# Kernel optimization log

Measured on AMD Instinct MI355X. Metric: run time of the kernel, lower is better.

The kernel has to match this reference:

```python
import jax, jax.numpy as jnp
import numpy as np

NHEAD = 8
D_MODEL = 256
B, L, NB = 16, 8192, 8


def setup_inputs() -> dict:
    key = jax.random.key(0)
    ks = jax.random.split(key, 8)
    x = jax.random.normal(ks[0], (B, L, D_MODEL), dtype=jnp.float32)
    mask = jax.random.randint(ks[1], (B, L), 0, 2) == 1  # bool, True = valid
    backend_id = jax.random.randint(ks[2], (B, L), 0, NB).astype(jnp.int32)
    query = 0.02 * jax.random.normal(ks[3], (1, 1, D_MODEL), dtype=jnp.float32)
    in_proj_weight = 0.02 * jax.random.normal(ks[4], (3 * D_MODEL, D_MODEL), dtype=jnp.float32)
    in_proj_bias = jnp.zeros((3 * D_MODEL,), dtype=jnp.float32)
    out_proj_weight = 0.02 * jax.random.normal(ks[5], (D_MODEL, D_MODEL), dtype=jnp.float32)
    out_proj_bias = jnp.zeros((D_MODEL,), dtype=jnp.float32)
    ln_gamma = jnp.ones((D_MODEL,), dtype=jnp.float32)
    ln_beta = jnp.zeros((D_MODEL,), dtype=jnp.float32)
    return {
        "x": x,
        "query": query,
        "in_proj_weight": in_proj_weight,
        "in_proj_bias": in_proj_bias,
        "out_proj_weight": out_proj_weight,
        "out_proj_bias": out_proj_bias,
        "ln_gamma": ln_gamma,
        "ln_beta": ln_beta,
        "mask": mask,
        "backend_id": backend_id,
        "n_backends_max": NB,
    }


def reference(x, query, in_proj_weight, in_proj_bias, out_proj_weight,
              out_proj_bias, ln_gamma, ln_beta, mask, backend_id, n_backends_max):
    Bs, Ls, D = x.shape
    H = NHEAD
    hd = D // H
    # Split packed torch in_proj into q/k/v projections.
    wq, wk, wv = jnp.split(in_proj_weight, 3, axis=0)
    bq, bk, bv = jnp.split(in_proj_bias, 3, axis=0)
    # Shared single query projected once (same for every batch/backend).
    q = (query[0, 0] @ wq.T + bq).reshape(H, hd)            # (H, hd)
    k = (x @ wk.T + bk).reshape(Bs, Ls, H, hd)              # (B, L, H, hd)
    v = (x @ wv.T + bv).reshape(Bs, Ls, H, hd)              # (B, L, H, hd)
    scores = jnp.einsum("hd,blhd->bhl", q, k) / jnp.sqrt(jnp.float32(hd))
    # Per-backend masks, vectorized over the backend axis n.
    b_ids = jnp.arange(n_backends_max, dtype=backend_id.dtype)
    b_mask = mask[None] & (backend_id[None] == b_ids[:, None, None])  # (NB, B, L)
    has_tokens = b_mask.any(axis=-1)                                   # (NB, B)
    safe_mask = jnp.where(has_tokens[:, :, None], b_mask, mask[None])  # fall back to full mask
    logits = jnp.where(safe_mask[:, :, None, :], scores[None], jnp.float32(-1e9))  # (NB,B,H,L)
    w = jax.nn.softmax(logits, axis=-1)
    ctx = jnp.einsum("nbhl,blhd->nbhd", w, v).reshape(n_backends_max, Bs, D)
    out = ctx @ out_proj_weight.T + out_proj_bias            # (NB, B, D)
    # LayerNorm over last dim.
    mu = out.mean(axis=-1, keepdims=True)
    var = out.var(axis=-1, keepdims=True)
    out = (out - mu) * jax.lax.rsqrt(var + 1e-5) * ln_gamma + ln_beta
    # Zero contexts for backends with no tokens.
    out = out * has_tokens[:, :, None].astype(out.dtype)
    return jnp.transpose(out, (1, 0, 2))                     # (B, NB, D)
```

## Files before the change

### kernel.cpp

```cpp
#include <hip/hip_runtime.h>
#include <cstdint>
#include <cstddef>

#define B_  16
#define L_  8192
#define D_  256
#define H_  8
#define NB_ 8

static const long OFF_QK   = 0;
static const long OFF_QB   = 2048;
static const long OFF_PART = 4096;

__global__ __launch_bounds__(256) void k_setup(const float* __restrict__ query,
                                               const float* __restrict__ W,
                                               const float* __restrict__ bias,
                                               float* __restrict__ ws) {
    __shared__ float q_s[256];
    int t = threadIdx.x;
    int h = blockIdx.x;
    float acc = bias[t];
    const float* wr = W + (long)t * 256;
    #pragma unroll 8
    for (int e = 0; e < 256; e += 4) {
        float4 qv = *(const float4*)(query + e);
        float4 wv = *(const float4*)(wr + e);
        acc += qv.x * wv.x + qv.y * wv.y + qv.z * wv.z + qv.w * wv.w;
    }
    q_s[t] = acc;
    __syncthreads();
    const float rs = 0.17677669529663687f;
    float s = 0.f;
    #pragma unroll 8
    for (int d = 0; d < 32; ++d) {
        int r = 256 + h * 32 + d;
        s += q_s[h * 32 + d] * W[(long)r * 256 + t];
    }
    ws[OFF_QK + h * 256 + t] = s * rs;
    if (t < 64) {
        float v = (t < 32) ? q_s[h * 32 + t] * bias[256 + h * 32 + t] : 0.f;
        v += __shfl_down(v, 16);
        v += __shfl_down(v, 8);
        v += __shfl_down(v, 4);
        v += __shfl_down(v, 2);
        v += __shfl_down(v, 1);
        if (t == 0) ws[OFF_QB + h] = v * rs;
    }
}

__device__ __forceinline__ float reduce_ep(float p0, float p1, float p2, float p3,
                                           float p4, float p5, float p6, float p7, int ep) {
    bool b1 = (ep & 1) != 0;
    float s0 = b1 ? p0 : p1, k0 = b1 ? p1 : p0;
    float s1 = b1 ? p2 : p3, k1 = b1 ? p3 : p2;
    float s2 = b1 ? p4 : p5, k2 = b1 ? p5 : p4;
    float s3 = b1 ? p6 : p7, k3 = b1 ? p7 : p6;
    float n0 = k0 + __shfl_xor(s0, 1);
    float n1 = k1 + __shfl_xor(s1, 1);
    float n2 = k2 + __shfl_xor(s2, 1);
    float n3 = k3 + __shfl_xor(s3, 1);
    bool b2 = (ep & 2) != 0;
    float t0s = b2 ? n0 : n1, t0k = b2 ? n1 : n0;
    float t1s = b2 ? n2 : n3, t1k = b2 ? n3 : n2;
    float m0 = t0k + __shfl_xor(t0s, 2);
    float m1 = t1k + __shfl_xor(t1s, 2);
    bool b4 = (ep & 4) != 0;
    float us = b4 ? m0 : m1, uk = b4 ? m1 : m0;
    return uk + __shfl_xor(us, 4);
}

template <int NCH>
__global__ __launch_bounds__(256) void k_pool(const float* __restrict__ x,
                                              const unsigned char* __restrict__ mask,
                                              const int* __restrict__ bid,
                                              const float* __restrict__ ws,
                                              float* __restrict__ part,
                                              float* __restrict__ pse) {
    const int CH = L_ / NCH;
    const int WLEN = CH / 4;
    __shared__ float red[4 * 2048];
    __shared__ float rse[4 * 8];

    int t = threadIdx.x;
    int widx = t >> 6, lane = t & 63;
    int ep = lane & 7;

    int blk = blockIdx.x;
    int b  = blk / (NB_ * NCH);
    int n  = (blk / NCH) % NB_;
    int ch = blk % NCH;

    const float* xb = x + (long)b * L_ * D_;
    const int*   bb = bid + (long)b * L_;

    float4 qk0 = *(const float4*)(ws + OFF_QK + 0 * 256 + lane * 4);
    float4 qk1 = *(const float4*)(ws + OFF_QK + 1 * 256 + lane * 4);
    float4 qk2 = *(const float4*)(ws + OFF_QK + 2 * 256 + lane * 4);
    float4 qk3 = *(const float4*)(ws + OFF_QK + 3 * 256 + lane * 4);
    float4 qk4 = *(const float4*)(ws + OFF_QK + 4 * 256 + lane * 4);
    float4 qk5 = *(const float4*)(ws + OFF_QK + 5 * 256 + lane * 4);
    float4 qk6 = *(const float4*)(ws + OFF_QK + 6 * 256 + lane * 4);
    float4 qk7 = *(const float4*)(ws + OFF_QK + 7 * 256 + lane * 4);
    float qbreg = ws[OFF_QB + ep];

    const int* mi = (const int*)mask;
    bool bytemode = __ballot((unsigned)mi[lane] > 1u) != 0ull;
    const unsigned char* mb_byte = mask + (long)b * L_;
    const int* mb_int = mi + (long)b * L_;

    float4 acc[8];
    #pragma unroll
    for (int h = 0; h < 8; ++h) acc[h] = make_float4(0.f, 0.f, 0.f, 0.f);
    float se = 0.f;

    int l0 = ch * CH + widx * WLEN;
    for (int w0 = l0; w0 < l0 + WLEN; w0 += 64) {
        int l = w0 + lane;
        bool valid = bytemode ? (mb_byte[l] != 0) : (mb_int[l] != 0);
        bool m = valid && (bb[l] == n);
        unsigned long long bal = __ballot(m);
        while (bal) {
            int i0 = __ffsll(bal) - 1; bal &= bal - 1;
            int i1 = -1;
            if (bal) { i1 = __ffsll(bal) - 1; bal &= bal - 1; }
            int tokA = w0 + i0;
            int tokB = w0 + (i1 >= 0 ? i1 : i0);
            float gB = (i1 >= 0) ? 1.f : 0.f;
            float4 xa = ((const float4*)(xb + (long)tokA * D_))[lane];
            float4 xc = ((const float4*)(xb + (long)tokB * D_))[lane];
            float pA0 = xa.x*qk0.x + xa.y*qk0.y + xa.z*qk0.z + xa.w*qk0.w;
            float pA1 = xa.x*qk1.x + xa.y*qk1.y + xa.z*qk1.z + xa.w*qk1.w;
            float pA2 = xa.x*qk2.x + xa.y*qk2.y + xa.z*qk2.z + xa.w*qk2.w;
            float pA3 = xa.x*qk3.x + xa.y*qk3.y + xa.z*qk3.z + xa.w*qk3.w;
            float pA4 = xa.x*qk4.x + xa.y*qk4.y + xa.z*qk4.z + xa.w*qk4.w;
            float pA5 = xa.x*qk5.x + xa.y*qk5.y + xa.z*qk5.z + xa.w*qk5.w;
            float pA6 = xa.x*qk6.x + xa.y*qk6.y + xa.z*qk6.z + xa.w*qk6.w;
            float pA7 = xa.x*qk7.x + xa.y*qk7.y + xa.z*qk7.z + xa.w*qk7.w;
            float pB0 = xc.x*qk0.x + xc.y*qk0.y + xc.z*qk0.z + xc.w*qk0.w;
            float pB1 = xc.x*qk1.x + xc.y*qk1.y + xc.z*qk1.z + xc.w*qk1.w;
            float pB2 = xc.x*qk2.x + xc.y*qk2.y + xc.z*qk2.z + xc.w*qk2.w;
            float pB3 = xc.x*qk3.x + xc.y*qk3.y + xc.z*qk3.z + xc.w*qk3.w;
            float pB4 = xc.x*qk4.x + xc.y*qk4.y + xc.z*qk4.z + xc.w*qk4.w;
            float pB5 = xc.x*qk5.x + xc.y*qk5.y + xc.z*qk5.z + xc.w*qk5.w;
            float pB6 = xc.x*qk6.x + xc.y*qk6.y + xc.z*qk6.z + xc.w*qk6.w;
            float pB7 = xc.x*qk7.x + xc.y*qk7.y + xc.z*qk7.z + xc.w*qk7.w;
            float sA = reduce_ep(pA0, pA1, pA2, pA3, pA4, pA5, pA6, pA7, ep);
            float sB = reduce_ep(pB0, pB1, pB2, pB3, pB4, pB5, pB6, pB7, ep);
            sA += __shfl_xor(sA, 8);  sB += __shfl_xor(sB, 8);
            sA += __shfl_xor(sA, 16); sB += __shfl_xor(sB, 16);
            sA += __shfl_xor(sA, 32); sB += __shfl_xor(sB, 32);
            float wA = __expf(sA + qbreg);
            float wB = __expf(sB + qbreg) * gB;
            se += wA + wB;
            {
                float a = __shfl(wA, 0), c = __shfl(wB, 0);
                acc[0].x += a*xa.x + c*xc.x; acc[0].y += a*xa.y + c*xc.y;
                acc[0].z += a*xa.z + c*xc.z; acc[0].w += a*xa.w + c*xc.w;
            }
            {
                float a = __shfl(wA, 1), c = __shfl(wB, 1);
                acc[1].x += a*xa.x + c*xc.x; acc[1].y += a*xa.y + c*xc.y;
                acc[1].z += a*xa.z + c*xc.z; acc[1].w += a*xa.w + c*xc.w;
            }
            {
                float a = __shfl(wA, 2), c = __shfl(wB, 2);
                acc[2].x += a*xa.x + c*xc.x; acc[2].y += a*xa.y + c*xc.y;
                acc[2].z += a*xa.z + c*xc.z; acc[2].w += a*xa.w + c*xc.w;
            }
            {
                float a = __shfl(wA, 3), c = __shfl(wB, 3);
                acc[3].x += a*xa.x + c*xc.x; acc[3].y += a*xa.y + c*xc.y;
                acc[3].z += a*xa.z + c*xc.z; acc[3].w += a*xa.w + c*xc.w;
            }
            {
                float a = __shfl(wA, 4), c = __shfl(wB, 4);
                acc[4].x += a*xa.x + c*xc.x; acc[4].y += a*xa.y + c*xc.y;
                acc[4].z += a*xa.z + c*xc.z; acc[4].w += a*xa.w + c*xc.w;
            }
            {
                float a = __shfl(wA, 5), c = __shfl(wB, 5);
                acc[5].x += a*xa.x + c*xc.x; acc[5].y += a*xa.y + c*xc.y;
                acc[5].z += a*xa.z + c*xc.z; acc[5].w += a*xa.w + c*xc.w;
            }
            {
                float a = __shfl(wA, 6), c = __shfl(wB, 6);
                acc[6].x += a*xa.x + c*xc.x; acc[6].y += a*xa.y + c*xc.y;
                acc[6].z += a*xa.z + c*xc.z; acc[6].w += a*xa.w + c*xc.w;
            }
            {
                float a = __shfl(wA, 7), c = __shfl(wB, 7);
                acc[7].x += a*xa.x + c*xc.x; acc[7].y += a*xa.y + c*xc.y;
                acc[7].z += a*xa.z + c*xc.z; acc[7].w += a*xa.w + c*xc.w;
            }
        }
    }

    #pragma unroll
    for (int h = 0; h < 8; ++h)
        *(float4*)(red + widx * 2048 + h * 256 + lane * 4) = acc[h];
    if (lane < 8) rse[widx * 8 + lane] = se;
    __syncthreads();
    long base = (long)blk * 2048;
    for (int idx = t; idx < 2048; idx += 256) {
        float s = red[idx] + red[2048 + idx] + red[4096 + idx] + red[6144 + idx];
        part[base + idx] = s;
    }
    if (t < 8) pse[(long)blk * 8 + t] = rse[t] + rse[8 + t] + rse[16 + t] + rse[24 + t];
}

template <int NCH>
__global__ __launch_bounds__(256) void k_epi(const float* __restrict__ part,
                                             const float* __restrict__ pse,
                                             const float* __restrict__ W,
                                             const float* __restrict__ ib,
                                             const float* __restrict__ Wo,
                                             const float* __restrict__ ob,
                                             const float* __restrict__ gamma,
                                             const float* __restrict__ beta,
                                             float* __restrict__ out) {
    __shared__ float pn[2048];
    __shared__ float ses[8];
    __shared__ float ctx_s[256];
    __shared__ float r1[4], r2[4];
    int n = blockIdx.x & 7, b = blockIdx.x >> 3;
    int t = threadIdx.x;
    int tbase = b * (NB_ * NCH) + n * NCH;
    if (t < 8) {
        float s = 0.f;
        for (int sub = 0; sub < NCH; ++sub) s += pse[(long)(tbase + sub) * 8 + t];
        ses[t] = s;
    }
    __syncthreads();
    bool has = ses[0] > 0.f;
    for (int j = 0; j < 8; ++j) {
        int idx = j * 256 + t;
        int h = idx >> 8;
        float s = 0.f;
        for (int sub = 0; sub < NCH; ++sub) s += part[(long)(tbase + sub) * 2048 + idx];
        pn[idx] = has ? s / ses[h] : 0.f;
    }
    __syncthreads();
    int h = t >> 5;
    float c = ib[512 + t];
    {
        const float* wr = W + (long)(512 + t) * 256;
        const float* ph = pn + h * 256;
        for (int e = 0; e < 256; e += 4) {
            float4 wv4 = *(const float4*)(wr + e);
            float4 pv4 = *(const float4*)(ph + e);
            c += wv4.x * pv4.x + wv4.y * pv4.y + wv4.z * pv4.z + wv4.w * pv4.w;
        }
    }
    ctx_s[t] = c;
    __syncthreads();
    float o = ob[t];
    {
        const float* wr = Wo + (long)t * 256;
        for (int d = 0; d < 256; d += 4) {
            float4 wv4 = *(const float4*)(wr + d);
            float4 cv4 = *(const float4*)(ctx_s + d);
            o += wv4.x * cv4.x + wv4.y * cv4.y + wv4.z * cv4.z + wv4.w * cv4.w;
        }
    }
    float s1 = o, s2 = o * o;
    #pragma unroll
    for (int off = 32; off >= 1; off >>= 1) {
        s1 += __shfl_down(s1, off);
        s2 += __shfl_down(s2, off);
    }
    if ((t & 63) == 0) { r1[t >> 6] = s1; r2[t >> 6] = s2; }
    __syncthreads();
    float S1 = r1[0] + r1[1] + r1[2] + r1[3];
    float S2 = r2[0] + r2[1] + r2[2] + r2[3];
    float mu = S1 * (1.f / 256.f);
    float var = S2 * (1.f / 256.f) - mu * mu;
    float rr = rsqrtf(var + 1e-5f);
    float res = ((o - mu) * rr * gamma[t] + beta[t]) * (has ? 1.f : 0.f);
    out[((long)b * 8 + n) * 256 + t] = res;
}

extern "C" void kernel_launch(void* const* d_in, const int* in_sizes, int n_in,
                              void* d_out, int out_size, void* d_ws, size_t ws_size,
                              hipStream_t stream) {
    const float* x     = (const float*)d_in[0];
    const float* query = (const float*)d_in[1];
    const float* W     = (const float*)d_in[2];
    const float* ib    = (const float*)d_in[3];
    const float* Wo    = (const float*)d_in[4];
    const float* ob    = (const float*)d_in[5];
    const float* gamma = (const float*)d_in[6];
    const float* beta  = (const float*)d_in[7];
    const unsigned char* mask = (const unsigned char*)d_in[8];
    const int* bid     = (const int*)d_in[9];
    float* out = (float*)d_out;
    float* ws  = (float*)d_ws;

    k_setup<<<8, 256, 0, stream>>>(query, W, ib, ws);

    auto need = [](long nch) {
        return (size_t)(OFF_PART + (long)B_ * NB_ * nch * (2048 + 8)) * sizeof(float);
    };
    float* part = ws + OFF_PART;
    if (ws_size >= need(16)) {
        const int NCH = 16;
        float* pse = part + (long)B_ * NB_ * NCH * 2048;
        k_pool<NCH><<<B_ * NB_ * NCH, 256, 0, stream>>>(x, mask, bid, ws, part, pse);
        k_epi<NCH><<<B_ * NB_, 256, 0, stream>>>(part, pse, W, ib, Wo, ob, gamma, beta, out);
    } else if (ws_size >= need(4)) {
        const int NCH = 4;
        float* pse = part + (long)B_ * NB_ * NCH * 2048;
        k_pool<NCH><<<B_ * NB_ * NCH, 256, 0, stream>>>(x, mask, bid, ws, part, pse);
        k_epi<NCH><<<B_ * NB_, 256, 0, stream>>>(part, pse, W, ib, Wo, ob, gamma, beta, out);
    } else {
        const int NCH = 1;
        float* pse = part + (long)B_ * NB_ * NCH * 2048;
        k_pool<NCH><<<B_ * NB_ * NCH, 256, 0, stream>>>(x, mask, bid, ws, part, pse);
        k_epi<NCH><<<B_ * NB_, 256, 0, stream>>>(part, pse, W, ib, Wo, ob, gamma, beta, out);
    }
}
```

Baseline: 68.39 us.

## Compact per-backend token lists via count/scan/fill before pooled gather

Result: slower. 73.62 us (+7.7%).

```diff
diff --git a/kernel.cpp b/kernel.cpp
--- a/kernel.cpp
+++ b/kernel.cpp
@@ -5,12 +5,16 @@
 #define B_  16
 #define L_  8192
 #define D_  256
-#define H_  8
 #define NB_ 8
+#define NW_ 128
 
 static const long OFF_QK   = 0;
 static const long OFF_QB   = 2048;
-static const long OFF_PART = 4096;
+static const long OFF_CNT  = 4096;
+static const long OFF_OFFS = 20480;
+static const long OFF_TOT  = 36864;
+static const long OFF_CIDX = 36992;
+static const long OFF_PART = 168064;
 
 __global__ __launch_bounds__(256) void k_setup(const float* __restrict__ query,
                                                const float* __restrict__ W,
@@ -45,6 +49,80 @@
         v += __shfl_down(v, 2);
         v += __shfl_down(v, 1);
         if (t == 0) ws[OFF_QB + h] = v * rs;
+    }
+}
+
+__global__ __launch_bounds__(256) void k_count(const unsigned char* __restrict__ mask,
+                                               const int* __restrict__ bid,
+                                               int* __restrict__ cnt) {
+    int widx = threadIdx.x >> 6, lane = threadIdx.x & 63;
+    int gw = blockIdx.x * 4 + widx;
+    int b = gw >> 7, w = gw & 127;
+    const int* mi = (const int*)mask;
+    bool bytemode = __ballot((unsigned)mi[lane] > 1u) != 0ull;
+    int tok = w * 64 + lane;
+    long gl = (long)b * L_ + tok;
+    bool valid = bytemode ? (mask[gl] != 0) : (mi[gl] != 0);
+    int nl = valid ? bid[gl] : NB_;
+    #pragma unroll
+    for (int n = 0; n < NB_; ++n) {
+        unsigned long long bn = __ballot(nl == n);
+        if (lane == n) cnt[(b * NB_ + n) * NW_ + w] = __popcll(bn);
+    }
+}
+
+__global__ __launch_bounds__(256) void k_scan(const int* __restrict__ cnt,
+                                              int* __restrict__ offs,
+                                              int* __restrict__ tot) {
+    __shared__ int c[16384];
+    __shared__ int sums[256];
+    int t = threadIdx.x;
+    for (int i = t; i < 16384; i += 256) c[i] = cnt[i];
+    __syncthreads();
+    int s = 0;
+    int base0 = t * 64;
+    for (int j = 0; j < 64; ++j) s += c[base0 + j];
+    sums[t] = s;
+    __syncthreads();
+    for (int st = 1; st < 256; st <<= 1) {
+        int v = (t >= st) ? sums[t - st] : 0;
+        __syncthreads();
+        sums[t] += v;
+        __syncthreads();
+    }
+    int run = sums[t] - s;
+    for (int j = 0; j < 64; ++j) {
+        offs[base0 + j] = run;
+        run += c[base0 + j];
+    }
+    if (t < 128) {
+        int hi = sums[2 * t + 1];
+        int lo = (t > 0) ? sums[2 * t - 1] : 0;
+        tot[t] = hi - lo;
+    }
+}
+
+__global__ __launch_bounds__(256) void k_fill(const unsigned char* __restrict__ mask,
+                                              const int* __restrict__ bid,
+                                              const int* __restrict__ offs,
+                                              int* __restrict__ cidx) {
+    int widx = threadIdx.x >> 6, lane = threadIdx.x & 63;
+    int gw = blockIdx.x * 4 + widx;
+    int b = gw >> 7, w = gw & 127;
+    const int* mi = (const int*)mask;
+    bool bytemode = __ballot((unsigned)mi[lane] > 1u) != 0ull;
+    int tok = w * 64 + lane;
+    long gl = (long)b * L_ + tok;
+    bool valid = bytemode ? (mask[gl] != 0) : (mi[gl] != 0);
+    int nl = valid ? bid[gl] : NB_;
+    unsigned long long ltmask = (1ull << lane) - 1ull;
+    #pragma unroll
+    for (int n = 0; n < NB_; ++n) {
+        unsigned long long bn = __ballot(nl == n);
+        if (nl == n) {
+            int ord = __popcll(bn & ltmask);
+            cidx[offs[(b * NB_ + n) * NW_ + w] + ord] = tok;
+        }
     }
 }
 
@@ -70,28 +148,33 @@
 }
 
 template <int NCH>
-__global__ __launch_bounds__(256) void k_pool(const float* __restrict__ x,
-                                              const unsigned char* __restrict__ mask,
-                                              const int* __restrict__ bid,
-                                              const float* __restrict__ ws,
-                                              float* __restrict__ part,
-                                              float* __restrict__ pse) {
-    const int CH = L_ / NCH;
-    const int WLEN = CH / 4;
+__global__ __launch_bounds__(256) void k_gather(const float* __restrict__ x,
+                                                const int* __restrict__ offs,
+                                                const int* __restrict__ tot,
+                                                const int* __restrict__ cidx,
+                                                const float* __restrict__ ws,
+                                                float* __restrict__ part,
+                                                float* __restrict__ pse) {
     __shared__ float red[4 * 2048];
     __shared__ float rse[4 * 8];
-
     int t = threadIdx.x;
     int widx = t >> 6, lane = t & 63;
     int ep = lane & 7;
 
     int blk = blockIdx.x;
-    int b  = blk / (NB_ * NCH);
-    int n  = (blk / NCH) % NB_;
+    int b = blk / (NB_ * NCH);
+    int n = (blk / NCH) % NB_;
     int ch = blk % NCH;
+    int bn = b * NB_ + n;
+    int start = offs[bn * NW_];
+    int cnt = tot[bn];
+    int c0 = start + (int)((long)cnt * ch / NCH);
+    int c1 = start + (int)((long)cnt * (ch + 1) / NCH);
+    int len = c1 - c0;
+    int w0 = c0 + (len * widx) / 4;
+    int w1 = c0 + (len * (widx + 1)) / 4;
 
     const float* xb = x + (long)b * L_ * D_;
-    const int*   bb = bid + (long)b * L_;
 
     float4 qk0 = *(const float4*)(ws + OFF_QK + 0 * 256 + lane * 4);
     float4 qk1 = *(const float4*)(ws + OFF_QK + 1 * 256 + lane * 4);
@@ -103,95 +186,81 @@
     float4 qk7 = *(const float4*)(ws + OFF_QK + 7 * 256 + lane * 4);
     float qbreg = ws[OFF_QB + ep];
 
-    const int* mi = (const int*)mask;
-    bool bytemode = __ballot((unsigned)mi[lane] > 1u) != 0ull;
-    const unsigned char* mb_byte = mask + (long)b * L_;
-    const int* mb_int = mi + (long)b * L_;
-
     float4 acc[8];
     #pragma unroll
     for (int h = 0; h < 8; ++h) acc[h] = make_float4(0.f, 0.f, 0.f, 0.f);
     float se = 0.f;
 
-    int l0 = ch * CH + widx * WLEN;
-    for (int w0 = l0; w0 < l0 + WLEN; w0 += 64) {
-        int l = w0 + lane;
-        bool valid = bytemode ? (mb_byte[l] != 0) : (mb_int[l] != 0);
-        bool m = valid && (bb[l] == n);
-        unsigned long long bal = __ballot(m);
-        while (bal) {
-            int i0 = __ffsll(bal) - 1; bal &= bal - 1;
-            int i1 = -1;
-            if (bal) { i1 = __ffsll(bal) - 1; bal &= bal - 1; }
-            int tokA = w0 + i0;
-            int tokB = w0 + (i1 >= 0 ? i1 : i0);
-            float gB = (i1 >= 0) ? 1.f : 0.f;
-            float4 xa = ((const float4*)(xb + (long)tokA * D_))[lane];
-            float4 xc = ((const float4*)(xb + (long)tokB * D_))[lane];
-            float pA0 = xa.x*qk0.x + xa.y*qk0.y + xa.z*qk0.z + xa.w*qk0.w;
-            float pA1 = xa.x*qk1.x + xa.y*qk1.y + xa.z*qk1.z + xa.w*qk1.w;
-            float pA2 = xa.x*qk2.x + xa.y*qk2.y + xa.z*qk2.z + xa.w*qk2.w;
-            float pA3 = xa.x*qk3.x + xa.y*qk3.y + xa.z*qk3.z + xa.w*qk3.w;
-            float pA4 = xa.x*qk4.x + xa.y*qk4.y + xa.z*qk4.z + xa.w*qk4.w;
-            float pA5 = xa.x*qk5.x + xa.y*qk5.y + xa.z*qk5.z + xa.w*qk5.w;
-            float pA6 = xa.x*qk6.x + xa.y*qk6.y + xa.z*qk6.z + xa.w*qk6.w;
-            float pA7 = xa.x*qk7.x + xa.y*qk7.y + xa.z*qk7.z + xa.w*qk7.w;
-            float pB0 = xc.x*qk0.x + xc.y*qk0.y + xc.z*qk0.z + xc.w*qk0.w;
-            float pB1 = xc.x*qk1.x + xc.y*qk1.y + xc.z*qk1.z + xc.w*qk1.w;
-            float pB2 = xc.x*qk2.x + xc.y*qk2.y + xc.z*qk2.z + xc.w*qk2.w;
-            float pB3 = xc.x*qk3.x + xc.y*qk3.y + xc.z*qk3.z + xc.w*qk3.w;
-            float pB4 = xc.x*qk4.x + xc.y*qk4.y + xc.z*qk4.z + xc.w*qk4.w;
-            float pB5 = xc.x*qk5.x + xc.y*qk5.y + xc.z*qk5.z + xc.w*qk5.w;
-            float pB6 = xc.x*qk6.x + xc.y*qk6.y + xc.z*qk6.z + xc.w*qk6.w;
-            float pB7 = xc.x*qk7.x + xc.y*qk7.y + xc.z*qk7.z + xc.w*qk7.w;
-            float sA = reduce_ep(pA0, pA1, pA2, pA3, pA4, pA5, pA6, pA7, ep);
-            float sB = reduce_ep(pB0, pB1, pB2, pB3, pB4, pB5, pB6, pB7, ep);
-            sA += __shfl_xor(sA, 8);  sB += __shfl_xor(sB, 8);
-            sA += __shfl_xor(sA, 16); sB += __shfl_xor(sB, 16);
-            sA += __shfl_xor(sA, 32); sB += __shfl_xor(sB, 32);
-            float wA = __expf(sA + qbreg);
-            float wB = __expf(sB + qbreg) * gB;
-            se += wA + wB;
-            {
-                float a = __shfl(wA, 0), c = __shfl(wB, 0);
-                acc[0].x += a*xa.x + c*xc.x; acc[0].y += a*xa.y + c*xc.y;
-                acc[0].z += a*xa.z + c*xc.z; acc[0].w += a*xa.w + c*xc.w;
-            }
-            {
-                float a = __shfl(wA, 1), c = __shfl(wB, 1);
-                acc[1].x += a*xa.x + c*xc.x; acc[1].y += a*xa.y + c*xc.y;
-                acc[1].z += a*xa.z + c*xc.z; acc[1].w += a*xa.w + c*xc.w;
-            }
-            {
-                float a = __shfl(wA, 2), c = __shfl(wB, 2);
-                acc[2].x += a*xa.x + c*xc.x; acc[2].y += a*xa.y + c*xc.y;
-                acc[2].z += a*xa.z + c*xc.z; acc[2].w += a*xa.w + c*xc.w;
-            }
-            {
-                float a = __shfl(wA, 3), c = __shfl(wB, 3);
-                acc[3].x += a*xa.x + c*xc.x; acc[3].y += a*xa.y + c*xc.y;
-                acc[3].z += a*xa.z + c*xc.z; acc[3].w += a*xa.w + c*xc.w;
-            }
-            {
-                float a = __shfl(wA, 4), c = __shfl(wB, 4);
-                acc[4].x += a*xa.x + c*xc.x; acc[4].y += a*xa.y + c*xc.y;
-                acc[4].z += a*xa.z + c*xc.z; acc[4].w += a*xa.w + c*xc.w;
-            }
-            {
-                float a = __shfl(wA, 5), c = __shfl(wB, 5);
-                acc[5].x += a*xa.x + c*xc.x; acc[5].y += a*xa.y + c*xc.y;
-                acc[5].z += a*xa.z + c*xc.z; acc[5].w += a*xa.w + c*xc.w;
-            }
-            {
-                float a = __shfl(wA, 6), c = __shfl(wB, 6);
-                acc[6].x += a*xa.x + c*xc.x; acc[6].y += a*xa.y + c*xc.y;
-                acc[6].z += a*xa.z + c*xc.z; acc[6].w += a*xa.w + c*xc.w;
-            }
-            {
-                float a = __shfl(wA, 7), c = __shfl(wB, 7);
-                acc[7].x += a*xa.x + c*xc.x; acc[7].y += a*xa.y + c*xc.y;
-                acc[7].z += a*xa.z + c*xc.z; acc[7].w += a*xa.w + c*xc.w;
-            }
+    for (int i = w0; i < w1; i += 2) {
+        int tokA = cidx[i];
+        bool hasB = (i + 1) < w1;
+        int tokB = cidx[hasB ? i + 1 : i];
+        float gB = hasB ? 1.f : 0.f;
+        float4 xa = ((const float4*)(xb + (long)tokA * D_))[lane];
+        float4 xc = ((const float4*)(xb + (long)tokB * D_))[lane];
+        float pA0 = xa.x*qk0.x + xa.y*qk0.y + xa.z*qk0.z + xa.w*qk0.w;
+        float pA1 = xa.x*qk1.x + xa.y*qk1.y + xa.z*qk1.z + xa.w*qk1.w;
+        float pA2 = xa.x*qk2.x + xa.y*qk2.y + xa.z*qk2.z + xa.w*qk2.w;
+        float pA3 = xa.x*qk3.x + xa.y*qk3.y + xa.z*qk3.z + xa.w*qk3.w;
+        float pA4 = xa.x*qk4.x + xa.y*qk4.y + xa.z*qk4.z + xa.w*qk4.w;
+        float pA5 = xa.x*qk5.x + xa.y*qk5.y + xa.z*qk5.z + xa.w*qk5.w;
+        float pA6 = xa.x*qk6.x + xa.y*qk6.y + xa.z*qk6.z + xa.w*qk6.w;
+        float pA7 = xa.x*qk7.x + xa.y*qk7.y + xa.z*qk7.z + xa.w*qk7.w;
+        float pB0 = xc.x*qk0.x + xc.y*qk0.y + xc.z*qk0.z + xc.w*qk0.w;
+        float pB1 = xc.x*qk1.x + xc.y*qk1.y + xc.z*qk1.z + xc.w*qk1.w;
+        float pB2 = xc.x*qk2.x + xc.y*qk2.y + xc.z*qk2.z + xc.w*qk2.w;
+        float pB3 = xc.x*qk3.x + xc.y*qk3.y + xc.z*qk3.z + xc.w*qk3.w;
+        float pB4 = xc.x*qk4.x + xc.y*qk4.y + xc.z*qk4.z + xc.w*qk4.w;
+        float pB5 = xc.x*qk5.x + xc.y*qk5.y + xc.z*qk5.z + xc.w*qk5.w;
+        float pB6 = xc.x*qk6.x + xc.y*qk6.y + xc.z*qk6.z + xc.w*qk6.w;
+        float pB7 = xc.x*qk7.x + xc.y*qk7.y + xc.z*qk7.z + xc.w*qk7.w;
+        float sA = reduce_ep(pA0, pA1, pA2, pA3, pA4, pA5, pA6, pA7, ep);
+        float sB = reduce_ep(pB0, pB1, pB2, pB3, pB4, pB5, pB6, pB7, ep);
+        sA += __shfl_xor(sA, 8);  sB += __shfl_xor(sB, 8);
+        sA += __shfl_xor(sA, 16); sB += __shfl_xor(sB, 16);
+        sA += __shfl_xor(sA, 32); sB += __shfl_xor(sB, 32);
+        float wA = __expf(sA + qbreg);
+        float wB = __expf(sB + qbreg) * gB;
+        se += wA + wB;
+        {
+            float a = __shfl(wA, 0), c = __shfl(wB, 0);
+            acc[0].x += a*xa.x + c*xc.x; acc[0].y += a*xa.y + c*xc.y;
+            acc[0].z += a*xa.z + c*xc.z; acc[0].w += a*xa.w + c*xc.w;
+        }
+        {
+            float a = __shfl(wA, 1), c = __shfl(wB, 1);
+            acc[1].x += a*xa.x + c*xc.x; acc[1].y += a*xa.y + c*xc.y;
+            acc[1].z += a*xa.z + c*xc.z; acc[1].w += a*xa.w + c*xc.w;
+        }
+        {
+            float a = __shfl(wA, 2), c = __shfl(wB, 2);
+            acc[2].x += a*xa.x + c*xc.x; acc[2].y += a*xa.y + c*xc.y;
+            acc[2].z += a*xa.z + c*xc.z; acc[2].w += a*xa.w + c*xc.w;
+        }
+        {
+            float a = __shfl(wA, 3), c = __shfl(wB, 3);
+            acc[3].x += a*xa.x + c*xc.x; acc[3].y += a*xa.y + c*xc.y;
+            acc[3].z += a*xa.z + c*xc.z; acc[3].w += a*xa.w + c*xc.w;
+        }
+        {
+            float a = __shfl(wA, 4), c = __shfl(wB, 4);
+            acc[4].x += a*xa.x + c*xc.x; acc[4].y += a*xa.y + c*xc.y;
+            acc[4].z += a*xa.z + c*xc.z; acc[4].w += a*xa.w + c*xc.w;
+        }
+        {
+            float a = __shfl(wA, 5), c = __shfl(wB, 5);
+            acc[5].x += a*xa.x + c*xc.x; acc[5].y += a*xa.y + c*xc.y;
+            acc[5].z += a*xa.z + c*xc.z; acc[5].w += a*xa.w + c*xc.w;
+        }
+        {
+            float a = __shfl(wA, 6), c = __shfl(wB, 6);
+            acc[6].x += a*xa.x + c*xc.x; acc[6].y += a*xa.y + c*xc.y;
+            acc[6].z += a*xa.z + c*xc.z; acc[6].w += a*xa.w + c*xc.w;
+        }
+        {
+            float a = __shfl(wA, 7), c = __shfl(wB, 7);
+            acc[7].x += a*xa.x + c*xc.x; acc[7].y += a*xa.y + c*xc.y;
+            acc[7].z += a*xa.z + c*xc.z; acc[7].w += a*xa.w + c*xc.w;
         }
     }
 
@@ -294,27 +363,28 @@
     const int* bid     = (const int*)d_in[9];
     float* out = (float*)d_out;
     float* ws  = (float*)d_ws;
+    int*   wsI = (int*)d_ws;
 
     k_setup<<<8, 256, 0, stream>>>(query, W, ib, ws);
+    k_count<<<512, 256, 0, stream>>>(mask, bid, wsI + OFF_CNT);
+    k_scan<<<1, 256, 0, stream>>>(wsI + OFF_CNT, wsI + OFF_OFFS, wsI + OFF_TOT);
+    k_fill<<<512, 256, 0, stream>>>(mask, bid, wsI + OFF_OFFS, wsI + OFF_CIDX);
 
     auto need = [](long nch) {
-        return (size_t)(OFF_PART + (long)B_ * NB_ * nch * (2048 + 8)) * sizeof(float);
+        return (size_t)(OFF_PART + nch * 128L * 2048 + nch * 128L * 8) * 4;
     };
     float* part = ws + OFF_PART;
-    if (ws_size >= need(16)) {
-        const int NCH = 16;
-        float* pse = part + (long)B_ * NB_ * NCH * 2048;
-        k_pool<NCH><<<B_ * NB_ * NCH, 256, 0, stream>>>(x, mask, bid, ws, part, pse);
-        k_epi<NCH><<<B_ * NB_, 256, 0, stream>>>(part, pse, W, ib, Wo, ob, gamma, beta, out);
-    } else if (ws_size >= need(4)) {
-        const int NCH = 4;
-        float* pse = part + (long)B_ * NB_ * NCH * 2048;
-        k_pool<NCH><<<B_ * NB_ * NCH, 256, 0, stream>>>(x, mask, bid, ws, part, pse);
+    if (ws_size >= need(8)) {
+        const int NCH = 8;
+        float* pse = part + (long)NCH * 128 * 2048;
+        k_gather<NCH><<<B_ * NB_ * NCH, 256, 0, stream>>>(
+            x, wsI + OFF_OFFS, wsI + OFF_TOT, wsI + OFF_CIDX, ws, part, pse);
         k_epi<NCH><<<B_ * NB_, 256, 0, stream>>>(part, pse, W, ib, Wo, ob, gamma, beta, out);
     } else {
         const int NCH = 1;
-        float* pse = part + (long)B_ * NB_ * NCH * 2048;
-        k_pool<NCH><<<B_ * NB_ * NCH, 256, 0, stream>>>(x, mask, bid, ws, part, pse);
+        float* pse = part + (long)NCH * 128 * 2048;
+        k_gather<NCH><<<B_ * NB_ * NCH, 256, 0, stream>>>(
+            x, wsI + OFF_OFFS, wsI + OFF_TOT, wsI + OFF_CIDX, ws, part, pse);
         k_epi<NCH><<<B_ * NB_, 256, 0, stream>>>(part, pse, W, ib, Wo, ob, gamma, beta, out);
     }
 }
```
